# Performance work log

Hardware: AMD Instinct MI355X
Metric: run time of the kernel (lower is better)

Reference implementation:

```python
import jax, jax.numpy as jnp
import numpy as np

CUTOFF = 5.0
N_GAUSS = 25
N_BASIS = 128
N_FILTERS = 128
N_BLOCKS = 3
MAX_Z = 5


def _linear(x, w, b):
    # w: (in, out)
    return x @ w + b


def setup_inputs() -> dict:
    key = jax.random.key(0)
    ks = jax.random.split(key, 24)
    B, N = 8, 256
    A, G, F, L = N_BASIS, N_GAUSS, N_FILTERS, N_BLOCKS
    s = 0.1
    inp = {
        "atomic_positions": jax.random.uniform(ks[0], (B, N, 3), dtype=jnp.float32) * 10.0,
        "atomic_numbers": jax.random.randint(ks[1], (B, N), 0, MAX_Z),
        "emb": jax.random.normal(ks[2], (MAX_Z, A), dtype=jnp.float32) * s,
        # stacked per-interaction-block parameters (leading dim = L blocks)
        "fw1_w": jax.random.normal(ks[3], (L, G, F), dtype=jnp.float32) * s,
        "fw1_b": jnp.zeros((L, F), jnp.float32),
        "fw2_w": jax.random.normal(ks[4], (L, F, F), dtype=jnp.float32) * s,
        "fw2_b": jnp.zeros((L, F), jnp.float32),
        "in2f_w": jax.random.normal(ks[5], (L, A, F), dtype=jnp.float32) * s,
        "in2f_b": jnp.zeros((L, F), jnp.float32),
        "f2out_w": jax.random.normal(ks[6], (L, F, A), dtype=jnp.float32) * s,
        "f2out_b": jnp.zeros((L, A), jnp.float32),
        "dense_w": jax.random.normal(ks[7], (L, A, A), dtype=jnp.float32) * s,
        "dense_b": jnp.zeros((L, A), jnp.float32),
        "e1_w": jax.random.normal(ks[8], (A, A), dtype=jnp.float32) * s,
        "e1_b": jnp.zeros((A,), jnp.float32),
        "e2_w": jax.random.normal(ks[9], (A, 1), dtype=jnp.float32) * s,
        "e2_b": jnp.zeros((1,), jnp.float32),
    }
    return inp


def reference(atomic_positions, atomic_numbers, emb,
              fw1_w, fw1_b, fw2_w, fw2_b, in2f_w, in2f_b,
              f2out_w, f2out_b, dense_w, dense_b,
              e1_w, e1_b, e2_w, e2_b):
    B, N, _ = atomic_positions.shape
    # static off-diagonal neighbor indices: nbh[i] = all j != i
    idx = np.arange(N)
    nbh = np.stack([np.delete(idx, i) for i in range(N)])  # (N, N-1)
    row = idx[:, None]                                      # (N, 1)

    x = emb[atomic_numbers]                                 # (B, N, A)

    # pairwise displacements gathered off-diagonal BEFORE the norm (avoids 0-dist)
    pair = atomic_positions[:, :, None, :] - atomic_positions[:, None, :, :]  # (B,N,N,3)
    pair_nb = pair[:, row, nbh, :]                          # (B, N, N-1, 3)
    r_ij = jnp.sqrt(jnp.sum(pair_nb * pair_nb, axis=-1))    # (B, N, N-1)

    centers = jnp.linspace(0.0, CUTOFF, N_GAUSS)
    variance = (centers[1] - centers[0]) ** 2
    f_ij = jnp.exp(-(0.5 / variance) * (r_ij[..., None] - centers) ** 2)  # (B,N,N-1,G)

    for l in range(N_BLOCKS):
        w = jnp.tanh(_linear(f_ij, fw1_w[l], fw1_b[l]))     # (B,N,N-1,F)
        w = _linear(w, fw2_w[l], fw2_b[l])
        y = _linear(x, in2f_w[l], in2f_b[l])                # (B,N,F)
        y_nb = y[:, nbh, :]                                 # gather neighbors (B,N,N-1,F)
        y = jnp.sum(y_nb * w, axis=2)                       # (B,N,F)
        y = jnp.tanh(_linear(y, f2out_w[l], f2out_b[l]))
        v = _linear(y, dense_w[l], dense_b[l])
        x = x + v

    x = jnp.tanh(_linear(x, e1_w, e1_b))
    x = _linear(x, e2_w, e2_b)                              # (B,N,1)
    return jnp.sum(x, axis=1)                               # (B,1)
```

## Files before the change

kernel.cpp:

```cpp
#include <hip/hip_runtime.h>
#include <hip/hip_bf16.h>

#define NATOM  256
#define NBASIS 128
#define NGAUSS 25
#define NFILT  128

typedef float f32x16 __attribute__((ext_vector_type(16)));
typedef short s16x8 __attribute__((ext_vector_type(8)));
typedef unsigned u32x4v __attribute__((ext_vector_type(4)));

union V8 { unsigned u[4]; s16x8 s; u32x4v q; };

__device__ inline unsigned cvt_pk_bf16(float lo, float hi) {
    unsigned d;
    asm("v_cvt_pk_bf16_f32 %0, %1, %2" : "=v"(d) : "v"(lo), "v"(hi));
    return d;
}
__device__ inline unsigned short f2bf(float v) {
    unsigned u = __builtin_bit_cast(unsigned, v);
    u = (u + 0x7FFF + ((u >> 16) & 1)) >> 16;
    return (unsigned short)u;
}
__device__ inline float bf2f(unsigned short u) {
    return __builtin_bit_cast(float, ((unsigned)u) << 16);
}
__device__ inline float fast_tanh(float x) {
    float e = __builtin_amdgcn_exp2f(x * 2.8853900817779268f);
    return 1.0f - 2.0f * __builtin_amdgcn_rcpf(e + 1.0f);
}
__device__ inline int yt_byte(int jj, int f) {
    int jt = jj >> 5, rho = jj & 31;
    int hh = (rho >> 2) & 1, r = (rho & 3) + ((rho >> 3) << 2);
    return (jt << 13) + (hh << 12) + ((((f << 5) + (r << 1)) ^ ((f & 7) << 4)));
}

__global__ __launch_bounds__(128) void k_prep(const float* __restrict__ fw1_w,
                                              const float* __restrict__ fw1_b,
                                              const float* __restrict__ fw2_w,
                                              const float* __restrict__ fw2_b,
                                              float* __restrict__ w0,
                                              unsigned short* __restrict__ W2sw,
                                              unsigned* __restrict__ a1g) {
    int role = blockIdx.x % 3, l = blockIdx.x / 3;
    int t = threadIdx.x;
    if (role == 0) {
        __shared__ float h[NFILT];
        int f = t;
        float acc = fw1_b[l * NFILT + f];
        #pragma unroll
        for (int g = 0; g < NGAUSS; ++g) {
            float c = (float)g * (5.0f / 24.0f);
            float f0 = __expf(-11.52f * c * c);
            acc += f0 * fw1_w[(l * NGAUSS + g) * NFILT + f];
        }
        h[f] = tanhf(acc);
        __syncthreads();
        float w = fw2_b[l * NFILT + f];
        for (int k = 0; k < NFILT; ++k) w += h[k] * fw2_w[(l * NFILT + k) * NFILT + f];
        w0[l * NFILT + f] = w;
    } else if (role == 1) {
        for (int e = t; e < 16384; e += 128) {
            int k = e >> 7, f = e & 127;
            unsigned short u = f2bf(fw2_w[l * 16384 + (k << 7) + f]);
            int byte = (((f << 8) + (k << 1)) ^ ((f & 7) << 4));
            *(unsigned short*)((char*)W2sw + (size_t)l * 32768 + byte) = u;
        }
    } else {
        if (t < 64) {
            int lane = t;
            int col = lane & 31, hi = lane >> 5;
            for (int idx = 0; idx < 32; ++idx) {
                int mt = idx >> 3, k2 = (idx >> 2) & 1, w = idx & 3;
                int k = (mt << 5) + col;
                int g0 = (k2 << 4) + (hi << 3) + (w << 1);
                int g1 = g0 + 1;
                float v0 = (g0 < 25) ? fw1_w[(l * 25 + g0) * 128 + k]
                                     : ((g0 == 25) ? fw1_b[l * 128 + k] : 0.0f);
                float v1 = (g1 < 25) ? fw1_w[(l * 25 + g1) * 128 + k]
                                     : ((g1 == 25) ? fw1_b[l * 128 + k] : 0.0f);
                a1g[l * 2048 + idx * 64 + lane] = cvt_pk_bf16(v0, v1);
            }
        }
    }
}

__global__ __launch_bounds__(256) void k_linear0(const float* __restrict__ emb,
                                                 const int* __restrict__ z,
                                                 const float* __restrict__ w,
                                                 const float* __restrict__ bias,
                                                 float* __restrict__ x,
                                                 unsigned short* __restrict__ y_t) {
    int half = threadIdx.x >> 7;
    int f = threadIdx.x & 127;
    int row = blockIdx.x * 2 + half;
    __shared__ float xs[2][NBASIS];
    float xv = emb[z[row] * NBASIS + f];
    x[row * NBASIS + f] = xv;
    xs[half][f] = xv;
    __syncthreads();
    float acc = bias[f];
    #pragma unroll 8
    for (int a = 0; a < NBASIS; ++a) acc += xs[half][a] * w[a * NFILT + f];
    int bb = row >> 8, rr = row & 255;
    int c = rr >> 6, jj = rr & 63;
    char* dst = (char*)y_t + (((size_t)((bb << 2) + c)) << 14) + yt_byte(jj, f);
    *(unsigned short*)dst = f2bf(acc);
}

__global__ __launch_bounds__(128) void k_ysum2(const unsigned short* __restrict__ y_t,
                                               float* __restrict__ ysum) {
    int b = blockIdx.x >> 3, fg = blockIdx.x & 7;
    int fl = threadIdx.x & 15, jg = threadIdx.x >> 4;
    int f = (fg << 4) + fl;
    float s = 0.0f;
    for (int q = 0; q < 32; ++q) {
        int j = (jg << 5) + q;
        int c = j >> 6, jj = j & 63;
        const char* p = (const char*)y_t + (((size_t)((b << 2) + c)) << 14) + yt_byte(jj, f);
        s += bf2f(*(const unsigned short*)p);
    }
    __shared__ float red[8][16];
    red[jg][fl] = s;
    __syncthreads();
    if (jg == 0) {
        float tot = 0.0f;
        #pragma unroll
        for (int k = 0; k < 8; ++k) tot += red[k][fl];
        ysum[(b << 7) + f] = tot;
    }
}

__global__ __launch_bounds__(256, 2) void k_cfconv_mfma(
    const float* __restrict__ pos,
    const unsigned short* __restrict__ y_t,
    const unsigned short* __restrict__ W2sw,
    const unsigned* __restrict__ a1g,
    const float* __restrict__ b2, const float* __restrict__ w0,
    const float* __restrict__ ysum, float* __restrict__ ynew)
{
    __shared__ unsigned short W2t[8192];
    __shared__ unsigned short ybufS[8192];
    __shared__ float px[NATOM], py[NATOM], pz[NATOM];

    const int t = threadIdx.x;
    const int b = blockIdx.x >> 7;
    const int r = blockIdx.x & 127;
    const int itile = r >> 1;
    const int fh = r & 1;
    const int wid = t >> 6;
    const int lane = t & 63;
    const int col = lane & 31;
    const int hi = lane >> 5;
    const int i = (itile << 2) + wid;
    const int swz = (col & 7) << 4;

    {
        const uint4* s4 = (const uint4*)W2sw + (fh << 10);
        uint4* d4 = (uint4*)W2t;
        #pragma unroll
        for (int e = 0; e < 4; ++e) d4[t + (e << 8)] = s4[t + (e << 8)];
        const float* pb = pos + (size_t)b * NATOM * 3;
        px[t] = pb[t * 3 + 0]; py[t] = pb[t * 3 + 1]; pz[t] = pb[t * 3 + 2];
    }

    unsigned a1w[4][2][4];
    #pragma unroll
    for (int mt = 0; mt < 4; ++mt)
      #pragma unroll
      for (int k2 = 0; k2 < 2; ++k2)
        #pragma unroll
        for (int w = 0; w < 4; ++w)
            a1w[mt][k2][w] = a1g[((((mt << 1) + k2) << 2) + w) * 64 + lane];

    __syncthreads();

    const float xi = px[i], yi2 = py[i], zi = pz[i];
    float accv[2] = {0.f, 0.f};

    for (int c = 0; c < 4; ++c) {
        {
            const uint4* src = (const uint4*)y_t + ((size_t)((b << 2) + c) << 10);
            uint4* dst = (uint4*)ybufS;
            #pragma unroll
            for (int e = 0; e < 4; ++e) dst[t + (e << 8)] = src[t + (e << 8)];
        }
        __syncthreads();

        #pragma unroll
        for (int jt = 0; jt < 2; ++jt) {
            int jcol = (c << 6) + (jt << 5) + col;
            float dxx = px[jcol] - xi, dyy = py[jcol] - yi2, dzz = pz[jcol] - zi;
            float rr = sqrtf(dxx * dxx + dyy * dyy + dzz * dzz);

            V8 b1f[2];
            #pragma unroll
            for (int k2 = 0; k2 < 2; ++k2)
              #pragma unroll
              for (int w = 0; w < 4; ++w) {
                int g0 = (k2 << 4) + (hi << 3) + (w << 1);
                int g1 = g0 + 1;
                float d0 = rr - (float)g0 * (5.0f / 24.0f);
                float d1v = rr - (float)g1 * (5.0f / 24.0f);
                float v0 = (g0 < 25) ? __builtin_amdgcn_exp2f(-16.619846812f * d0 * d0)
                                     : ((g0 == 25) ? 1.0f : 0.0f);
                float v1 = (g1 < 25) ? __builtin_amdgcn_exp2f(-16.619846812f * d1v * d1v)
                                     : ((g1 == 25) ? 1.0f : 0.0f);
                b1f[k2].u[w] = cvt_pk_bf16(v0, v1);
              }

            unsigned a2[8][4];
            #pragma unroll
            for (int mt = 0; mt < 4; ++mt) {
                f32x16 d1;
                #pragma unroll
                for (int q = 0; q < 16; ++q) d1[q] = 0.0f;
                V8 A0, A1;
                #pragma unroll
                for (int w = 0; w < 4; ++w) { A0.u[w] = a1w[mt][0][w]; A1.u[w] = a1w[mt][1][w]; }
                d1 = __builtin_amdgcn_mfma_f32_32x32x16_bf16(A0.s, b1f[0].s, d1, 0, 0, 0);
                d1 = __builtin_amdgcn_mfma_f32_32x32x16_bf16(A1.s, b1f[1].s, d1, 0, 0, 0);
                #pragma unroll
                for (int q = 0; q < 16; ++q) d1[q] = fast_tanh(d1[q]);
                unsigned p[4][2];
                #pragma unroll
                for (int q = 0; q < 4; ++q) {
                    p[q][0] = cvt_pk_bf16(d1[4 * q + 0], d1[4 * q + 1]);
                    p[q][1] = cvt_pk_bf16(d1[4 * q + 2], d1[4 * q + 3]);
                }
                #pragma unroll
                for (int k2 = 0; k2 < 2; ++k2) {
                    unsigned pa0 = p[2 * k2][0], pb0 = p[2 * k2 + 1][0];
                    unsigned pa1 = p[2 * k2][1], pb1 = p[2 * k2 + 1][1];
                    unsigned xa0 = (unsigned)__shfl_xor((int)pa0, 32, 64);
                    unsigned xb0 = (unsigned)__shfl_xor((int)pb0, 32, 64);
                    unsigned xa1 = (unsigned)__shfl_xor((int)pa1, 32, 64);
                    unsigned xb1 = (unsigned)__shfl_xor((int)pb1, 32, 64);
                    int ks = 2 * mt + k2;
                    a2[ks][0] = hi ? xb0 : pa0;
                    a2[ks][1] = hi ? xb1 : pa1;
                    a2[ks][2] = hi ? pb0 : xa0;
                    a2[ks][3] = hi ? pb1 : xa1;
                }
            }

            #pragma unroll
            for (int ntl = 0; ntl < 2; ++ntl) {
                int fc = (fh << 6) + (ntl << 5) + col;
                int fcl = (ntl << 5) + col;
                f32x16 c2;
                #pragma unroll
                for (int q = 0; q < 16; ++q) c2[q] = 0.0f;
                #pragma unroll
                for (int ks = 0; ks < 8; ++ks) {
                    int byte = (((fcl << 8) + (ks << 5) + (hi << 4)) ^ swz);
                    V8 bf; bf.q = *(const u32x4v*)((const char*)W2t + byte);
                    V8 af;
                    af.u[0] = a2[ks][0]; af.u[1] = a2[ks][1];
                    af.u[2] = a2[ks][2]; af.u[3] = a2[ks][3];
                    c2 = __builtin_amdgcn_mfma_f32_32x32x16_bf16(af.s, bf.s, c2, 0, 0, 0);
                }
                const char* yb = (const char*)ybufS + (jt << 13) + (hi << 12);
                V8 y0; y0.q = *(const u32x4v*)(yb + (((fc << 5) + 0) ^ swz));
                V8 y1; y1.q = *(const u32x4v*)(yb + (((fc << 5) + 16) ^ swz));
                #pragma unroll
                for (int w = 0; w < 8; ++w) {
                    unsigned uw = (w < 4) ? y0.u[w] : y1.u[w - 4];
                    float ylo = __builtin_bit_cast(float, uw << 16);
                    float yhv = __builtin_bit_cast(float, uw & 0xFFFF0000u);
                    accv[ntl] += c2[2 * w] * ylo;
                    accv[ntl] += c2[2 * w + 1] * yhv;
                }
            }
        }
        __syncthreads();
    }

    #pragma unroll
    for (int ntl = 0; ntl < 2; ++ntl) {
        float a = accv[ntl] + __shfl_xor(accv[ntl], 32, 64);
        if (hi == 0) {
            int f = (fh << 6) + (ntl << 5) + col;
            int cc = i >> 6, jj = i & 63;
            const char* p = (const char*)y_t + (((size_t)((b << 2) + cc)) << 14) + yt_byte(jj, f);
            float yv = bf2f(*(const unsigned short*)p);
            size_t o = ((size_t)((b << 8) + i) << 7) + f;
            ynew[o] = a + b2[f] * ysum[(b << 7) + f] - yv * w0[f];
        }
    }
}

__global__ __launch_bounds__(128) void k_postlin(const float* __restrict__ ynew,
                                                 const float* __restrict__ f2w,
                                                 const float* __restrict__ f2b,
                                                 const float* __restrict__ dw,
                                                 const float* __restrict__ db,
                                                 float* __restrict__ x,
                                                 const float* __restrict__ w3,
                                                 const float* __restrict__ b3,
                                                 const float* __restrict__ e2w,
                                                 unsigned short* __restrict__ y_t,
                                                 float* __restrict__ rsum,
                                                 int mode) {
    int row = blockIdx.x;
    int f = threadIdx.x;
    __shared__ float yr[NFILT], y2[NFILT], xs[NFILT];
    __shared__ float ws2[2];
    yr[f] = ynew[row * NFILT + f];
    __syncthreads();
    float acc = f2b[f];
    #pragma unroll 8
    for (int a = 0; a < NFILT; ++a) acc += yr[a] * f2w[a * NBASIS + f];
    y2[f] = tanhf(acc);
    __syncthreads();
    float v = db[f];
    #pragma unroll 8
    for (int a = 0; a < NFILT; ++a) v += y2[a] * dw[a * NBASIS + f];
    float xn = x[row * NBASIS + f] + v;
    x[row * NBASIS + f] = xn;
    xs[f] = xn;
    __syncthreads();
    float acc3 = b3[f];
    #pragma unroll 8
    for (int a = 0; a < NBASIS; ++a) acc3 += xs[a] * w3[a * NFILT + f];
    if (mode == 0) {
        int bb = row >> 8, rr = row & 255;
        int c = rr >> 6, jj = rr & 63;
        char* dst = (char*)y_t + (((size_t)((bb << 2) + c)) << 14) + yt_byte(jj, f);
        *(unsigned short*)dst = f2bf(acc3);
    } else {
        float p = tanhf(acc3) * e2w[f];
        #pragma unroll
        for (int off = 32; off > 0; off >>= 1) p += __shfl_down(p, off, 64);
        if ((f & 63) == 0) ws2[f >> 6] = p;
        __syncthreads();
        if (f == 0) rsum[row] = ws2[0] + ws2[1];
    }
}

__global__ __launch_bounds__(256) void k_head_final(const float* __restrict__ rowsum,
                                                    const float* __restrict__ e2b,
                                                    float* __restrict__ out) {
    int b = blockIdx.x;
    int t = threadIdx.x;
    __shared__ float ws2[4];
    float p = rowsum[b * NATOM + t];
    #pragma unroll
    for (int off = 32; off > 0; off >>= 1) p += __shfl_down(p, off, 64);
    if ((t & 63) == 0) ws2[t >> 6] = p;
    __syncthreads();
    if (t == 0) out[b] = ws2[0] + ws2[1] + ws2[2] + ws2[3] + 256.0f * e2b[0];
}

extern "C" void kernel_launch(void* const* d_in, const int* in_sizes, int n_in,
                              void* d_out, int out_size, void* d_ws, size_t ws_size,
                              hipStream_t stream) {
    const float* pos    = (const float*)d_in[0];
    const int*   z      = (const int*)d_in[1];
    const float* emb    = (const float*)d_in[2];
    const float* fw1_w  = (const float*)d_in[3];
    const float* fw1_b  = (const float*)d_in[4];
    const float* fw2_w  = (const float*)d_in[5];
    const float* fw2_b  = (const float*)d_in[6];
    const float* in2f_w = (const float*)d_in[7];
    const float* in2f_b = (const float*)d_in[8];
    const float* f2o_w  = (const float*)d_in[9];
    const float* f2o_b  = (const float*)d_in[10];
    const float* dns_w  = (const float*)d_in[11];
    const float* dns_b  = (const float*)d_in[12];
    const float* e1w    = (const float*)d_in[13];
    const float* e1b    = (const float*)d_in[14];
    const float* e2w    = (const float*)d_in[15];
    const float* e2b    = (const float*)d_in[16];

    float* ws   = (float*)d_ws;
    float* x    = ws;
    float* ynew = x + 262144;
    float* w0   = ynew + 262144;
    float* rsum = w0 + 384;
    float* ysum = rsum + 2048;
    unsigned* a1g = (unsigned*)(ysum + 1024);
    unsigned short* W2sw = (unsigned short*)(a1g + 6144);
    unsigned short* y_t  = (unsigned short*)((float*)W2sw + 24576);

    float* out = (float*)d_out;

    k_prep<<<9, 128, 0, stream>>>(fw1_w, fw1_b, fw2_w, fw2_b, w0, W2sw, a1g);
    k_linear0<<<1024, 256, 0, stream>>>(emb, z, in2f_w, in2f_b, x, y_t);
    k_ysum2<<<64, 128, 0, stream>>>(y_t, ysum);

    for (int l = 0; l < 3; ++l) {
        k_cfconv_mfma<<<1024, 256, 0, stream>>>(pos, y_t,
                                                W2sw + l * 16384,
                                                a1g + l * 2048,
                                                fw2_b + l * NFILT,
                                                w0 + l * NFILT, ysum, ynew);
        if (l < 2) {
            k_postlin<<<2048, 128, 0, stream>>>(ynew, f2o_w + l * 16384,
                                                f2o_b + l * 128,
                                                dns_w + l * 16384,
                                                dns_b + l * 128, x,
                                                in2f_w + (l + 1) * 16384,
                                                in2f_b + (l + 1) * 128,
                                                e2w, y_t, rsum, 0);
            k_ysum2<<<64, 128, 0, stream>>>(y_t, ysum);
        } else {
            k_postlin<<<2048, 128, 0, stream>>>(ynew, f2o_w + l * 16384,
                                                f2o_b + l * 128,
                                                dns_w + l * 16384,
                                                dns_b + l * 128, x,
                                                e1w, e1b,
                                                e2w, y_t, rsum, 1);
        }
    }
    k_head_final<<<8, 256, 0, stream>>>(rsum, e2b, out);
}
```

Before: 258.9 us.

## Compute all filters per block and split neighbors across wave halves

Each cfconv block now covers all 128 filters for four atoms instead of one filter half, so the Gaussian expansion and first filter layer are computed once per pair rather than twice. The neighbor range is split between two groups of four waves in a 512-thread block, and their partial sums are combined through shared memory. This adds LDS usage (full W2 plus two y buffers), more accumulators per wave and an extra barrier, which may lower occupancy.

Measured after the change: 282.9 us. 9.3% more time.

```diff
diff --git a/kernel.cpp b/kernel.cpp
--- a/kernel.cpp
+++ b/kernel.cpp
@@ -131,7 +131,7 @@
     }
 }
 
-__global__ __launch_bounds__(256, 2) void k_cfconv_mfma(
+__global__ __launch_bounds__(512, 2) void k_cfconv_mfma(
     const float* __restrict__ pos,
     const unsigned short* __restrict__ y_t,
     const unsigned short* __restrict__ W2sw,
@@ -139,29 +139,31 @@
     const float* __restrict__ b2, const float* __restrict__ w0,
     const float* __restrict__ ysum, float* __restrict__ ynew)
 {
-    __shared__ unsigned short W2t[8192];
-    __shared__ unsigned short ybufS[8192];
+    __shared__ unsigned short W2t[16384];
+    __shared__ unsigned short ybA[8192];
+    __shared__ unsigned short ybB[8192];
     __shared__ float px[NATOM], py[NATOM], pz[NATOM];
 
     const int t = threadIdx.x;
-    const int b = blockIdx.x >> 7;
-    const int r = blockIdx.x & 127;
-    const int itile = r >> 1;
-    const int fh = r & 1;
+    const int b = blockIdx.x >> 6;
+    const int ibase = (blockIdx.x & 63) << 2;
     const int wid = t >> 6;
     const int lane = t & 63;
     const int col = lane & 31;
     const int hi = lane >> 5;
-    const int i = (itile << 2) + wid;
+    const int half = wid >> 2;
+    const int i = ibase + (wid & 3);
     const int swz = (col & 7) << 4;
 
     {
-        const uint4* s4 = (const uint4*)W2sw + (fh << 10);
+        const uint4* s4 = (const uint4*)W2sw;
         uint4* d4 = (uint4*)W2t;
         #pragma unroll
-        for (int e = 0; e < 4; ++e) d4[t + (e << 8)] = s4[t + (e << 8)];
-        const float* pb = pos + (size_t)b * NATOM * 3;
-        px[t] = pb[t * 3 + 0]; py[t] = pb[t * 3 + 1]; pz[t] = pb[t * 3 + 2];
+        for (int e = 0; e < 4; ++e) d4[t + (e << 9)] = s4[t + (e << 9)];
+        if (t < 256) {
+            const float* pb = pos + (size_t)b * NATOM * 3;
+            px[t] = pb[t * 3 + 0]; py[t] = pb[t * 3 + 1]; pz[t] = pb[t * 3 + 2];
+        }
     }
 
     unsigned a1w[4][2][4];
@@ -176,20 +178,25 @@
     __syncthreads();
 
     const float xi = px[i], yi2 = py[i], zi = pz[i];
-    float accv[2] = {0.f, 0.f};
-
-    for (int c = 0; c < 4; ++c) {
+    float accv[4] = {0.f, 0.f, 0.f, 0.f};
+
+    for (int s = 0; s < 2; ++s) {
         {
-            const uint4* src = (const uint4*)y_t + ((size_t)((b << 2) + c) << 10);
-            uint4* dst = (uint4*)ybufS;
-            #pragma unroll
-            for (int e = 0; e < 4; ++e) dst[t + (e << 8)] = src[t + (e << 8)];
+            const uint4* srcA = (const uint4*)y_t + ((size_t)b << 12) + (s << 10);
+            const uint4* srcB = srcA + (2 << 10);
+            uint4* dA = (uint4*)ybA; uint4* dB = (uint4*)ybB;
+            dA[t] = srcA[t];
+            dA[t + 512] = srcA[t + 512];
+            dB[t] = srcB[t];
+            dB[t + 512] = srcB[t + 512];
         }
         __syncthreads();
+        const unsigned short* myb = half ? ybB : ybA;
+        const int cs = (half << 1) + s;
 
         #pragma unroll
         for (int jt = 0; jt < 2; ++jt) {
-            int jcol = (c << 6) + (jt << 5) + col;
+            int jcol = (cs << 6) + (jt << 5) + col;
             float dxx = px[jcol] - xi, dyy = py[jcol] - yi2, dzz = pz[jcol] - zi;
             float rr = sqrtf(dxx * dxx + dyy * dyy + dzz * dzz);
 
@@ -245,22 +252,21 @@
             }
 
             #pragma unroll
-            for (int ntl = 0; ntl < 2; ++ntl) {
-                int fc = (fh << 6) + (ntl << 5) + col;
-                int fcl = (ntl << 5) + col;
+            for (int nt = 0; nt < 4; ++nt) {
+                int fc = (nt << 5) + col;
                 f32x16 c2;
                 #pragma unroll
                 for (int q = 0; q < 16; ++q) c2[q] = 0.0f;
                 #pragma unroll
                 for (int ks = 0; ks < 8; ++ks) {
-                    int byte = (((fcl << 8) + (ks << 5) + (hi << 4)) ^ swz);
+                    int byte = (((fc << 8) + (ks << 5) + (hi << 4)) ^ swz);
                     V8 bf; bf.q = *(const u32x4v*)((const char*)W2t + byte);
                     V8 af;
                     af.u[0] = a2[ks][0]; af.u[1] = a2[ks][1];
                     af.u[2] = a2[ks][2]; af.u[3] = a2[ks][3];
                     c2 = __builtin_amdgcn_mfma_f32_32x32x16_bf16(af.s, bf.s, c2, 0, 0, 0);
                 }
-                const char* yb = (const char*)ybufS + (jt << 13) + (hi << 12);
+                const char* yb = (const char*)myb + (jt << 13) + (hi << 12);
                 V8 y0; y0.q = *(const u32x4v*)(yb + (((fc << 5) + 0) ^ swz));
                 V8 y1; y1.q = *(const u32x4v*)(yb + (((fc << 5) + 16) ^ swz));
                 #pragma unroll
@@ -268,19 +274,27 @@
                     unsigned uw = (w < 4) ? y0.u[w] : y1.u[w - 4];
                     float ylo = __builtin_bit_cast(float, uw << 16);
                     float yhv = __builtin_bit_cast(float, uw & 0xFFFF0000u);
-                    accv[ntl] += c2[2 * w] * ylo;
-                    accv[ntl] += c2[2 * w + 1] * yhv;
+                    accv[nt] += c2[2 * w] * ylo;
+                    accv[nt] += c2[2 * w + 1] * yhv;
                 }
             }
         }
         __syncthreads();
     }
 
+    float* red = (float*)ybA;
     #pragma unroll
-    for (int ntl = 0; ntl < 2; ++ntl) {
-        float a = accv[ntl] + __shfl_xor(accv[ntl], 32, 64);
-        if (hi == 0) {
-            int f = (fh << 6) + (ntl << 5) + col;
+    for (int nt = 0; nt < 4; ++nt) {
+        float a = accv[nt] + __shfl_xor(accv[nt], 32, 64);
+        if (hi == 0) red[(((wid << 2) + nt) << 5) + col] = a;
+    }
+    __syncthreads();
+    if (half == 0 && hi == 0) {
+        #pragma unroll
+        for (int nt = 0; nt < 4; ++nt) {
+            int f = (nt << 5) + col;
+            float a = red[(((wid << 2) + nt) << 5) + col]
+                    + red[((((wid + 4) << 2) + nt) << 5) + col];
             int cc = i >> 6, jj = i & 63;
             const char* p = (const char*)y_t + (((size_t)((b << 2) + cc)) << 14) + yt_byte(jj, f);
             float yv = bf2f(*(const unsigned short*)p);
@@ -390,11 +404,11 @@
     k_ysum2<<<64, 128, 0, stream>>>(y_t, ysum);
 
     for (int l = 0; l < 3; ++l) {
-        k_cfconv_mfma<<<1024, 256, 0, stream>>>(pos, y_t,
-                                                W2sw + l * 16384,
-                                                a1g + l * 2048,
-                                                fw2_b + l * NFILT,
-                                                w0 + l * NFILT, ysum, ynew);
+        k_cfconv_mfma<<<512, 512, 0, stream>>>(pos, y_t,
+                                               W2sw + l * 16384,
+                                               a1g + l * 2048,
+                                               fw2_b + l * NFILT,
+                                               w0 + l * NFILT, ysum, ynew);
         if (l < 2) {
             k_postlin<<<2048, 128, 0, stream>>>(ynew, f2o_w + l * 16384,
                                                 f2o_b + l * 128,
```
